# Performance work log

Measured on AMD Instinct MI355X. Metric: run time of the kernel, lower is better.

Reference implementation:

```python
import jax, jax.numpy as jnp
import numpy as np

CUTOFF = 5.0   # radius cutoff r
N_BASIS = 20   # radial Bessel basis size
P = 9          # polynomial cutoff degree
BOX = 40.0     # box edge length (Angstrom) for atom positions
N_ATOMS = 2048


def setup_inputs() -> dict:
    key = jax.random.key(0)
    # atoms uniformly distributed in a cubic box -> realistic sparse radius graph
    pos = jax.random.uniform(key, (N_ATOMS, 3), dtype=jnp.float32) * BOX
    return {"pos": pos}


def reference(pos):
    """EdgeEmbedding.forward (cell=None, batch=None), dense-masked jit form.

    Returns:
      dist_edge: [N, N, n_basis]  envelope(d/r) * bessel(d/r), zero outside radius/diagonal
      dir_edge:  [N, N, 3]        unit displacement vectors, zero outside radius/diagonal
      mask:      [N, N] bool      valid-edge mask (replaces dynamic edge_index)
    """
    r, p, n_basis = CUTOFF, P, N_BASIS
    n = pos.shape[0]
    disp = pos[:, None, :] - pos[None, :, :]          # [N, N, 3], disp[i,j] = pos[i]-pos[j]
    dist = jnp.sqrt(jnp.sum(disp * disp, axis=-1))    # [N, N]
    eye = jnp.eye(n, dtype=bool)
    mask = (dist < r) & (~eye)                        # RadiusGraph: i != j and |d| < r

    safe_dist = jnp.where(mask, dist, 1.0)            # avoid 0-div on diagonal / masked
    dir_edge = jnp.where(mask[..., None], disp / safe_dist[..., None], 0.0)  # ScaledNorm dir
    x = safe_dist / r                                 # ScaledNorm scaled distance

    # PolynomialCutoff: 1 - .5(p+1)(p+2)x^p + p(p+2)x^(p+1) - .5 p(p+1)x^(p+2)
    xp = x ** p
    env = 1.0 - 0.5 * (p + 1) * (p + 2) * xp + p * (p + 2) * xp * x - 0.5 * p * (p + 1) * xp * x * x

    # RadialBesselLayer: sin(k*pi*x)/x for k = 1..n_basis
    freqs = jnp.arange(1, n_basis + 1, dtype=pos.dtype) * jnp.pi  # [n_basis]
    bessel = jnp.sin(freqs * x[..., None]) / x[..., None]         # [N, N, n_basis]

    dist_edge = jnp.where(mask[..., None], env[..., None] * bessel, 0.0)
    return (dist_edge, dir_edge, mask)
```

## Files before the change

### kernel.cpp

```cpp
#include <hip/hip_runtime.h>
#include <math.h>


#define NATOMS 2048
#define NBASIS 20
#define RCUT   5.0f
#define PAIRS_PER_BLOCK 64
#define BLOCK_THREADS   320

__global__ __launch_bounds__(BLOCK_THREADS) void edge_embed_kernel(
    const float* __restrict__ pos, float* __restrict__ out)
{
    const int t = threadIdx.x;
    const int blocksPerRow = NATOMS / PAIRS_PER_BLOCK;
    const int i  = blockIdx.x / blocksPerRow;
    const int j0 = (blockIdx.x % blocksPerRow) * PAIRS_PER_BLOCK;

    const int p = t / 5;
    const int q = t - 5 * p;
    const int j = j0 + p;

    const float xi = pos[3 * i + 0], yi = pos[3 * i + 1], zi = pos[3 * i + 2];
    const float xj = pos[3 * j + 0], yj = pos[3 * j + 1], zj = pos[3 * j + 2];
    const float dx = xi - xj, dy = yi - yj, dz = zi - zj;
    float d2;
    {
#pragma clang fp contract(off)
        d2 = (dx * dx + dy * dy) + dz * dz;
    }
    const float dist = sqrtf(d2);
    const bool m = (dist < RCUT) && (i != j);

    float4 v = make_float4(0.0f, 0.0f, 0.0f, 0.0f);
    if (m) {
        const float x  = dist * (1.0f / RCUT);
        const float x2 = x * x, x4 = x2 * x2, x8 = x4 * x4, x9 = x8 * x;
        const float env = 1.0f - 55.0f * x9 + 99.0f * x9 * x - 45.0f * x9 * x2;
        const float scale = env / x;
        const float theta = 3.14159265358979323846f * x;
        const float k0 = (float)(4 * q + 1);
        const float s0 = sinf(k0 * theta);
        const float s1 = sinf((k0 + 1.0f) * theta);
        const float twoc = 2.0f * cosf(theta);
        const float s2 = twoc * s1 - s0;
        const float s3 = twoc * s2 - s1;
        v = make_float4(scale * s0, scale * s1, scale * s2, scale * s3);
    }

    const long long pair = (long long)i * NATOMS + j;
    float4* __restrict__ de = (float4*)out;
    de[pair * 5 + q] = v;

    if (t < PAIRS_PER_BLOCK) {
        const int j2 = j0 + t;
        const float xj2 = pos[3 * j2 + 0], yj2 = pos[3 * j2 + 1], zj2 = pos[3 * j2 + 2];
        const float ex = xi - xj2, ey = yi - yj2, ez = zi - zj2;
        float e2;
        {
#pragma clang fp contract(off)
            e2 = (ex * ex + ey * ey) + ez * ez;
        }
        const float ed = sqrtf(e2);
        const bool m2 = (ed < RCUT) && (i != j2);
        float ox = 0.0f, oy = 0.0f, oz = 0.0f, mv = 0.0f;
        if (m2) { ox = ex / ed; oy = ey / ed; oz = ez / ed; mv = 1.0f; }
        const long long pair2 = (long long)i * NATOMS + j2;
        float* __restrict__ dir = out + (long long)NATOMS * NATOMS * NBASIS + pair2 * 3;
        float* __restrict__ mk  = out + (long long)NATOMS * NATOMS * (NBASIS + 3) + pair2;
        dir[0] = ox; dir[1] = oy; dir[2] = oz;
        *mk = mv;
    }
}

extern "C" void kernel_launch(void* const* d_in, const int* in_sizes, int n_in,
                              void* d_out, int out_size, void* d_ws, size_t ws_size,
                              hipStream_t stream) {
    const float* pos = (const float*)d_in[0];
    float* out = (float*)d_out;
    edge_embed_kernel<<<dim3(NATOMS * (NATOMS / PAIRS_PER_BLOCK)), dim3(BLOCK_THREADS), 0, stream>>>(pos, out);
}
```

Measured before the change: 395.8 us.

## Split into bulk nontemporal zero-fill and sparse in-cutoff edge kernel

Replaces the dense per-pair kernel with two launches: a vectorized nontemporal zero-fill of the whole output, then a kernel where each thread handles one pair and returns early unless it lies within the cutoff. Only valid edges compute the Bessel/envelope terms and write values, so transcendental work and uncoalesced writes are skipped for the vast majority of pairs. It adds a second launch and a full output write pass, and the sparse pass overwrites some lines already zeroed. The direction is now computed with a reciprocal multiply instead of division.

Result: slower. 455.3 us (+15.0%).

```diff
diff --git a/kernel.cpp b/kernel.cpp
--- a/kernel.cpp
+++ b/kernel.cpp
@@ -5,20 +5,34 @@
 #define NATOMS 2048
 #define NBASIS 20
 #define RCUT   5.0f
-#define PAIRS_PER_BLOCK 64
-#define BLOCK_THREADS   320
 
-__global__ __launch_bounds__(BLOCK_THREADS) void edge_embed_kernel(
+#define DIR_OFF   ((long long)NATOMS * NATOMS * NBASIS)
+#define MASK_OFF  ((long long)NATOMS * NATOMS * (NBASIS + 3))
+
+typedef float f32x4 __attribute__((ext_vector_type(4)));
+
+#define ZBLOCKS  4096
+#define ZTHREADS 256
+#define ZITERS   24
+
+__global__ __launch_bounds__(ZTHREADS) void edge_zero_kernel(f32x4* __restrict__ out)
+{
+    const long long tid    = (long long)blockIdx.x * blockDim.x + threadIdx.x;
+    const long long stride = (long long)gridDim.x * blockDim.x;
+    const f32x4 z = (f32x4)(0.0f);
+#pragma unroll
+    for (int k = 0; k < ZITERS; ++k) {
+        __builtin_nontemporal_store(z, out + tid + (long long)k * stride);
+    }
+}
+
+#define EBLOCK 256
+
+__global__ __launch_bounds__(EBLOCK) void edge_sparse_kernel(
     const float* __restrict__ pos, float* __restrict__ out)
 {
-    const int t = threadIdx.x;
-    const int blocksPerRow = NATOMS / PAIRS_PER_BLOCK;
-    const int i  = blockIdx.x / blocksPerRow;
-    const int j0 = (blockIdx.x % blocksPerRow) * PAIRS_PER_BLOCK;
-
-    const int p = t / 5;
-    const int q = t - 5 * p;
-    const int j = j0 + p;
+    const int i = blockIdx.x >> 3;
+    const int j = ((blockIdx.x & 7) << 8) | threadIdx.x;
 
     const float xi = pos[3 * i + 0], yi = pos[3 * i + 1], zi = pos[3 * i + 2];
     const float xj = pos[3 * j + 0], yj = pos[3 * j + 1], zj = pos[3 * j + 2];
@@ -29,53 +43,38 @@
         d2 = (dx * dx + dy * dy) + dz * dz;
     }
     const float dist = sqrtf(d2);
-    const bool m = (dist < RCUT) && (i != j);
+    if (!((dist < RCUT) && (i != j))) return;
 
-    float4 v = make_float4(0.0f, 0.0f, 0.0f, 0.0f);
-    if (m) {
-        const float x  = dist * (1.0f / RCUT);
-        const float x2 = x * x, x4 = x2 * x2, x8 = x4 * x4, x9 = x8 * x;
-        const float env = 1.0f - 55.0f * x9 + 99.0f * x9 * x - 45.0f * x9 * x2;
-        const float scale = env / x;
-        const float theta = 3.14159265358979323846f * x;
-        const float k0 = (float)(4 * q + 1);
-        const float s0 = sinf(k0 * theta);
-        const float s1 = sinf((k0 + 1.0f) * theta);
-        const float twoc = 2.0f * cosf(theta);
-        const float s2 = twoc * s1 - s0;
-        const float s3 = twoc * s2 - s1;
-        v = make_float4(scale * s0, scale * s1, scale * s2, scale * s3);
-    }
+    const float x  = dist * (1.0f / RCUT);
+    const float x2 = x * x, x4 = x2 * x2, x8 = x4 * x4, x9 = x8 * x;
+    const float env   = 1.0f - 55.0f * x9 + 99.0f * x9 * x - 45.0f * x9 * x2;
+    const float scale = env / x;
+    const float theta = 3.14159265358979323846f * x;
+    const float twoc  = 2.0f * cosf(theta);
 
     const long long pair = (long long)i * NATOMS + j;
     float4* __restrict__ de = (float4*)out;
-    de[pair * 5 + q] = v;
+#pragma unroll
+    for (int g = 0; g < 5; ++g) {
+        const float k0 = (float)(4 * g + 1);
+        const float s0 = sinf(k0 * theta);
+        const float s1 = sinf((k0 + 1.0f) * theta);
+        const float s2 = twoc * s1 - s0;
+        const float s3 = twoc * s2 - s1;
+        de[pair * 5 + g] = make_float4(scale * s0, scale * s1, scale * s2, scale * s3);
+    }
 
-    if (t < PAIRS_PER_BLOCK) {
-        const int j2 = j0 + t;
-        const float xj2 = pos[3 * j2 + 0], yj2 = pos[3 * j2 + 1], zj2 = pos[3 * j2 + 2];
-        const float ex = xi - xj2, ey = yi - yj2, ez = zi - zj2;
-        float e2;
-        {
-#pragma clang fp contract(off)
-            e2 = (ex * ex + ey * ey) + ez * ez;
-        }
-        const float ed = sqrtf(e2);
-        const bool m2 = (ed < RCUT) && (i != j2);
-        float ox = 0.0f, oy = 0.0f, oz = 0.0f, mv = 0.0f;
-        if (m2) { ox = ex / ed; oy = ey / ed; oz = ez / ed; mv = 1.0f; }
-        const long long pair2 = (long long)i * NATOMS + j2;
-        float* __restrict__ dir = out + (long long)NATOMS * NATOMS * NBASIS + pair2 * 3;
-        float* __restrict__ mk  = out + (long long)NATOMS * NATOMS * (NBASIS + 3) + pair2;
-        dir[0] = ox; dir[1] = oy; dir[2] = oz;
-        *mk = mv;
-    }
+    const float inv = 1.0f / dist;
+    float* __restrict__ dir = out + DIR_OFF + pair * 3;
+    dir[0] = dx * inv; dir[1] = dy * inv; dir[2] = dz * inv;
+    out[MASK_OFF + pair] = 1.0f;
 }
 
 extern "C" void kernel_launch(void* const* d_in, const int* in_sizes, int n_in,
                               void* d_out, int out_size, void* d_ws, size_t ws_size,
                               hipStream_t stream) {
     const float* pos = (const float*)d_in[0];
-    float* out = (float*)d_out;
-    edge_embed_kernel<<<dim3(NATOMS * (NATOMS / PAIRS_PER_BLOCK)), dim3(BLOCK_THREADS), 0, stream>>>(pos, out);
+    edge_zero_kernel<<<dim3(ZBLOCKS), dim3(ZTHREADS), 0, stream>>>((f32x4*)d_out);
+    edge_sparse_kernel<<<dim3(NATOMS * (NATOMS / EBLOCK)), dim3(EBLOCK), 0, stream>>>(
+        pos, (float*)d_out);
 }
```
